# Optimization experiments

Hardware: AMD Instinct MI355X
Metric: run time of the kernel (lower is better)

Reference implementation:

```python
import jax, jax.numpy as jnp
import numpy as np

B, N_IN, D = 2, 262144, 32
N_OUT, K, NK = 65536, 4, 9
MIN_DIST = 0.01


def setup_inputs() -> dict:
    key = jax.random.key(0)
    k1, k2, k3, k4 = jax.random.split(key, 4)
    x_level_in = jax.random.normal(k1, (B, N_IN, D), dtype=jnp.float32)
    coords_in = jax.random.uniform(k2, (2, B, N_IN), dtype=jnp.float32)
    coords_out = jax.random.uniform(k3, (2, B, N_OUT, K), dtype=jnp.float32)
    neighbor_idx = jax.random.randint(k4, (B, N_OUT, K, NK), 0, N_IN)
    sigma = jnp.ones((D,), dtype=jnp.float32) * (MIN_DIST * 200.0)
    return {
        "x_level_in": x_level_in,
        "coords_in": coords_in,
        "coords_out": coords_out,
        "sigma": sigma,
        "neighbor_idx": neighbor_idx,
    }


def reference(x_level_in, coords_in, coords_out, sigma, neighbor_idx):
    # x_level_in: [B, N_in, D]; coords_in: [2, B, N_in]
    # coords_out: [2, B, N_out, K]; neighbor_idx: [B, N_out, K, NK]; sigma: [D]
    b = jnp.arange(x_level_in.shape[0])[:, None, None, None]  # batch index broadcaster
    # gather neighbor coordinates across the input grid: [2, B, N_out, K, NK]
    nb_coords = coords_in[:, b, neighbor_idx]
    # squared euclidean distance in (lon, lat): [B, N_out, K, NK]
    d2 = jnp.sum((coords_out[..., None] - nb_coords) ** 2, axis=0)
    # per-channel Gaussian/RBF weights: [B, N_out, K, NK, D]
    w = jnp.exp(-d2[..., None] / (2.0 * sigma ** 2))
    # gather neighbor features: [B, N_out, K, NK, D]
    feats = x_level_in[b, neighbor_idx]
    # normalized weighted aggregate over the NK neighbors: [B, N_out, K, D]
    num = jnp.sum(w * feats, axis=3)
    den = jnp.sum(w, axis=3) + 1e-9
    x = num / den
    # flatten (N_out, K) -> sequence dim, as in forward's final view
    return x.reshape(x.shape[0], -1, x.shape[-1])
```

## Files before the change

kernel.cpp:

```cpp
#include <hip/hip_runtime.h>
#include <hip/hip_fp16.h>

constexpr int B        = 2;
constexpr int N_IN     = 262144;
constexpr int D        = 32;
constexpr int N_OUT    = 65536;
constexpr int K        = 4;
constexpr int NK       = 9;
constexpr int P        = B * N_OUT * K;
constexpr int PPB      = N_OUT * K;
constexpr size_t XTOT  = (size_t)B * N_IN * D;

typedef _Float16 half2v __attribute__((ext_vector_type(2)));
typedef _Float16 half8v __attribute__((ext_vector_type(8)));
typedef float    f4v    __attribute__((ext_vector_type(4)));

__global__ __launch_bounds__(256) void cvt_fp16_kernel(
    const float* __restrict__ x, _Float16* __restrict__ xh)
{
    const size_t i = (size_t)(blockIdx.x * 256 + threadIdx.x) * 8;
    const float4 a = *reinterpret_cast<const float4*>(x + i);
    const float4 b = *reinterpret_cast<const float4*>(x + i + 4);
    half8v h;
    h[0] = (_Float16)a.x; h[1] = (_Float16)a.y;
    h[2] = (_Float16)a.z; h[3] = (_Float16)a.w;
    h[4] = (_Float16)b.x; h[5] = (_Float16)b.y;
    h[6] = (_Float16)b.z; h[7] = (_Float16)b.w;
    *reinterpret_cast<half8v*>(xh + i) = h;
}

__global__ __launch_bounds__(256) void pack_coords_kernel(
    const float* __restrict__ cin, half2v* __restrict__ cp)
{
    const int i = blockIdx.x * 256 + threadIdx.x;
    half2v h;
    h[0] = (_Float16)cin[i];
    h[1] = (_Float16)cin[B * N_IN + i];
    cp[i] = h;
}

__global__ __launch_bounds__(256) void projection_kernel_h(
    const _Float16* __restrict__ xh,
    const half2v*   __restrict__ cpack,
    const float*    __restrict__ coords_out,
    const float*    __restrict__ sigma,
    const int*      __restrict__ nidx,
    float*          __restrict__ out)
{
    const int bid   = blockIdx.x;
    const int xcd   = bid & 7;
    const int j     = bid >> 3;
    const int batch = xcd >> 2;
    const int bbi   = j * 4 + (xcd & 3);
    const int point = batch * PPB + bbi * 64 + (threadIdx.x >> 2);
    const int h     = threadIdx.x & 3;

    const int cbase = batch * N_IN;

    const float cox = __builtin_nontemporal_load(coords_out + point);
    const float coy = __builtin_nontemporal_load(coords_out + P + point);

    const float4 sg0 = *reinterpret_cast<const float4*>(sigma + h * 8);
    const float4 sg1 = *reinterpret_cast<const float4*>(sigma + h * 8 + 4);
    float s[8];
    s[0] = 1.0f / (2.0f * sg0.x * sg0.x); s[1] = 1.0f / (2.0f * sg0.y * sg0.y);
    s[2] = 1.0f / (2.0f * sg0.z * sg0.z); s[3] = 1.0f / (2.0f * sg0.w * sg0.w);
    s[4] = 1.0f / (2.0f * sg1.x * sg1.x); s[5] = 1.0f / (2.0f * sg1.y * sg1.y);
    s[6] = 1.0f / (2.0f * sg1.z * sg1.z); s[7] = 1.0f / (2.0f * sg1.w * sg1.w);
    bool uni = true;
    #pragma unroll
    for (int k = 1; k < 8; ++k) uni = uni && (s[k] == s[0]);

    int idxs[NK];
    const int* __restrict__ ip = nidx + (size_t)point * NK;
    #pragma unroll
    for (int t = 0; t < NK; ++t) idxs[t] = __builtin_nontemporal_load(ip + t);

    half2v c[NK];
    #pragma unroll
    for (int t = 0; t < NK; ++t) c[t] = cpack[cbase + idxs[t]];

    half8v f[NK];
    #pragma unroll
    for (int t = 0; t < NK; ++t)
        f[t] = *reinterpret_cast<const half8v*>(
            xh + (size_t)(cbase + idxs[t]) * D + h * 8);

    float num[8];
    #pragma unroll
    for (int k = 0; k < 8; ++k) num[k] = 0.f;

    float den[8];
    #pragma unroll
    for (int k = 0; k < 8; ++k) den[k] = 0.f;

    if (uni) {
        #pragma unroll
        for (int t = 0; t < NK; ++t) {
            const float dx = cox - (float)c[t][0];
            const float dy = coy - (float)c[t][1];
            const float w  = __expf(-(dx * dx + dy * dy) * s[0]);
            den[0] += w;
            #pragma unroll
            for (int k = 0; k < 8; ++k) num[k] += w * (float)f[t][k];
        }
        #pragma unroll
        for (int k = 1; k < 8; ++k) den[k] = den[0];
    } else {
        #pragma unroll
        for (int t = 0; t < NK; ++t) {
            const float dx = cox - (float)c[t][0];
            const float dy = coy - (float)c[t][1];
            const float d2 = dx * dx + dy * dy;
            #pragma unroll
            for (int k = 0; k < 8; ++k) {
                const float w = __expf(-d2 * s[k]);
                num[k] += w * (float)f[t][k];
                den[k] += w;
            }
        }
    }

    float* op = out + (size_t)point * D + h * 8;
    f4v o0, o1;
    o0.x = num[0] / (den[0] + 1e-9f); o0.y = num[1] / (den[1] + 1e-9f);
    o0.z = num[2] / (den[2] + 1e-9f); o0.w = num[3] / (den[3] + 1e-9f);
    o1.x = num[4] / (den[4] + 1e-9f); o1.y = num[5] / (den[5] + 1e-9f);
    o1.z = num[6] / (den[6] + 1e-9f); o1.w = num[7] / (den[7] + 1e-9f);
    __builtin_nontemporal_store(o0, reinterpret_cast<f4v*>(op));
    __builtin_nontemporal_store(o1, reinterpret_cast<f4v*>(op + 4));
}

__global__ __launch_bounds__(256) void projection_kernel_f32(
    const float* __restrict__ x,
    const float* __restrict__ coords_in,
    const float* __restrict__ coords_out,
    const float* __restrict__ sigma,
    const int*   __restrict__ nidx,
    float*       __restrict__ out)
{
    const int tid   = blockIdx.x * 256 + threadIdx.x;
    const int point = tid >> 3;
    const int q     = tid & 7;
    const int b     = point / PPB;
    const int cbase = b * N_IN;

    const float cox = coords_out[point];
    const float coy = coords_out[P + point];

    const float4 sg = *reinterpret_cast<const float4*>(sigma + q * 4);
    const float s0 = 1.0f / (2.0f * sg.x * sg.x);
    const float s1 = 1.0f / (2.0f * sg.y * sg.y);
    const float s2 = 1.0f / (2.0f * sg.z * sg.z);
    const float s3 = 1.0f / (2.0f * sg.w * sg.w);

    float4 num = make_float4(0.f, 0.f, 0.f, 0.f);
    float4 den = make_float4(0.f, 0.f, 0.f, 0.f);
    const int* __restrict__ ip = nidx + (size_t)point * NK;

    #pragma unroll
    for (int nk = 0; nk < NK; ++nk) {
        const int idx = ip[nk];
        const float cx = coords_in[cbase + idx];
        const float cy = coords_in[B * N_IN + cbase + idx];
        const float dx = cox - cx;
        const float dy = coy - cy;
        const float d2 = dx * dx + dy * dy;
        const float4 f = *reinterpret_cast<const float4*>(
            x + (size_t)(cbase + idx) * D + q * 4);
        const float w0 = __expf(-d2 * s0);
        const float w1 = __expf(-d2 * s1);
        const float w2 = __expf(-d2 * s2);
        const float w3 = __expf(-d2 * s3);
        num.x += w0 * f.x;  den.x += w0;
        num.y += w1 * f.y;  den.y += w1;
        num.z += w2 * f.z;  den.z += w2;
        num.w += w3 * f.w;  den.w += w3;
    }

    float4 o;
    o.x = num.x / (den.x + 1e-9f);
    o.y = num.y / (den.y + 1e-9f);
    o.z = num.z / (den.z + 1e-9f);
    o.w = num.w / (den.w + 1e-9f);
    *reinterpret_cast<float4*>(out + (size_t)point * D + q * 4) = o;
}

extern "C" void kernel_launch(void* const* d_in, const int* in_sizes, int n_in,
                              void* d_out, int out_size, void* d_ws, size_t ws_size,
                              hipStream_t stream) {
    const float* x      = (const float*)d_in[0];
    const float* cin    = (const float*)d_in[1];
    const float* cout_  = (const float*)d_in[2];
    const float* sigma  = (const float*)d_in[3];
    const int*   nidx   = (const int*)  d_in[4];
    float*       outp   = (float*)d_out;

    const int block = 256;

    const size_t xh_bytes = XTOT * sizeof(_Float16);
    const size_t cp_bytes = (size_t)B * N_IN * sizeof(half2v);

    if (ws_size >= xh_bytes + cp_bytes) {
        _Float16* xh = (_Float16*)d_ws;
        half2v*   cp = (half2v*)((char*)d_ws + xh_bytes);
        cvt_fp16_kernel<<<(int)(XTOT / 8 / block), block, 0, stream>>>(x, xh);
        pack_coords_kernel<<<(B * N_IN) / block, block, 0, stream>>>(cin, cp);
        const int grid_main = (P * 4) / block;
        projection_kernel_h<<<grid_main, block, 0, stream>>>(
            xh, cp, cout_, sigma, nidx, outp);
    } else {
        const int grid_main = (P * 8) / block;
        projection_kernel_f32<<<grid_main, block, 0, stream>>>(
            x, cin, cout_, sigma, nidx, outp);
    }
}
```

Measured before the change: 218.5 us.

## Fuse prep kernels and restructure gather into phased per-thread full-row accumulation

Merges the fp16 conversion and coordinate packing into one prep kernel. The main kernel now gives each thread two whole output points (all 32 channels) instead of a quarter point. It computes scalar weights once per neighbor, then gathers feature rows in four phases keyed on the index range, with block barriers between phases so that concurrent blocks touch a narrower slice of the fp16 feature array and get better L2 locality. The grid is fixed at 1024 blocks with a launch-bounds occupancy hint. The cost is higher register pressure (64 accumulators), fewer threads in flight, and divergent branches within each phase.

```diff
diff --git a/kernel.cpp b/kernel.cpp
--- a/kernel.cpp
+++ b/kernel.cpp
@@ -10,36 +10,77 @@
 constexpr int P        = B * N_OUT * K;
 constexpr int PPB      = N_OUT * K;
 constexpr size_t XTOT  = (size_t)B * N_IN * D;
+constexpr int NPH      = 4;
 
 typedef _Float16 half2v __attribute__((ext_vector_type(2)));
 typedef _Float16 half8v __attribute__((ext_vector_type(8)));
 typedef float    f4v    __attribute__((ext_vector_type(4)));
 
-__global__ __launch_bounds__(256) void cvt_fp16_kernel(
-    const float* __restrict__ x, _Float16* __restrict__ xh)
-{
-    const size_t i = (size_t)(blockIdx.x * 256 + threadIdx.x) * 8;
-    const float4 a = *reinterpret_cast<const float4*>(x + i);
-    const float4 b = *reinterpret_cast<const float4*>(x + i + 4);
+__global__ __launch_bounds__(256) void prep_kernel(
+    const float* __restrict__ x,   _Float16* __restrict__ xh,
+    const float* __restrict__ cin, half2v*   __restrict__ cp)
+{
+    const int tid  = blockIdx.x * 256 + threadIdx.x;
+    const size_t i = (size_t)tid * 8;
+    const f4v a = __builtin_nontemporal_load(reinterpret_cast<const f4v*>(x + i));
+    const f4v b = __builtin_nontemporal_load(reinterpret_cast<const f4v*>(x + i) + 1);
     half8v h;
-    h[0] = (_Float16)a.x; h[1] = (_Float16)a.y;
-    h[2] = (_Float16)a.z; h[3] = (_Float16)a.w;
-    h[4] = (_Float16)b.x; h[5] = (_Float16)b.y;
-    h[6] = (_Float16)b.z; h[7] = (_Float16)b.w;
+    h[0] = (_Float16)a[0]; h[1] = (_Float16)a[1];
+    h[2] = (_Float16)a[2]; h[3] = (_Float16)a[3];
+    h[4] = (_Float16)b[0]; h[5] = (_Float16)b[1];
+    h[6] = (_Float16)b[2]; h[7] = (_Float16)b[3];
     *reinterpret_cast<half8v*>(xh + i) = h;
-}
-
-__global__ __launch_bounds__(256) void pack_coords_kernel(
-    const float* __restrict__ cin, half2v* __restrict__ cp)
-{
-    const int i = blockIdx.x * 256 + threadIdx.x;
-    half2v h;
-    h[0] = (_Float16)cin[i];
-    h[1] = (_Float16)cin[B * N_IN + i];
-    cp[i] = h;
-}
-
-__global__ __launch_bounds__(256) void projection_kernel_h(
+    if (tid < B * N_IN) {
+        half2v c;
+        c[0] = (_Float16)cin[tid];
+        c[1] = (_Float16)cin[B * N_IN + tid];
+        cp[tid] = c;
+    }
+}
+
+__device__ void slow_point(
+    int p, int cbase, const _Float16* __restrict__ xb,
+    const half2v* __restrict__ cpack, const float* __restrict__ coords_out,
+    const float* __restrict__ sigma, const int* __restrict__ nidx,
+    float* __restrict__ out)
+{
+    const float cox = coords_out[p];
+    const float coy = coords_out[P + p];
+    const int* __restrict__ ip = nidx + (size_t)p * NK;
+    int id[NK]; float d2[NK];
+    #pragma unroll
+    for (int t = 0; t < NK; ++t) id[t] = ip[t];
+    #pragma unroll
+    for (int t = 0; t < NK; ++t) {
+        const half2v c = cpack[cbase + id[t]];
+        const float dx = cox - (float)c[0], dy = coy - (float)c[1];
+        d2[t] = dx * dx + dy * dy;
+    }
+    for (int q = 0; q < 4; ++q) {
+        float n[8], d[8], s[8];
+        #pragma unroll
+        for (int k = 0; k < 8; ++k) {
+            n[k] = 0.f; d[k] = 0.f;
+            const float g = sigma[q * 8 + k];
+            s[k] = 1.0f / (2.0f * g * g);
+        }
+        #pragma unroll
+        for (int t = 0; t < NK; ++t) {
+            const half8v f = *reinterpret_cast<const half8v*>(xb + id[t] * D + q * 8);
+            #pragma unroll
+            for (int k = 0; k < 8; ++k) {
+                const float w = __expf(-d2[t] * s[k]);
+                n[k] += w * (float)f[k];
+                d[k] += w;
+            }
+        }
+        #pragma unroll
+        for (int k = 0; k < 8; ++k)
+            out[(size_t)p * D + q * 8 + k] = n[k] / (d[k] + 1e-9f);
+    }
+}
+
+__global__ __launch_bounds__(256, 4) void projection_phase_kernel(
     const _Float16* __restrict__ xh,
     const half2v*   __restrict__ cpack,
     const float*    __restrict__ coords_out,
@@ -49,86 +90,116 @@
 {
     const int bid   = blockIdx.x;
     const int xcd   = bid & 7;
-    const int j     = bid >> 3;
     const int batch = xcd >> 2;
-    const int bbi   = j * 4 + (xcd & 3);
-    const int point = batch * PPB + bbi * 64 + (threadIdx.x >> 2);
-    const int h     = threadIdx.x & 3;
-
+    const int wb    = (bid >> 3) * 4 + (xcd & 3);
+    const int p0    = batch * PPB + wb * 512 + threadIdx.x;
+    const int p1    = p0 + 256;
     const int cbase = batch * N_IN;
-
-    const float cox = __builtin_nontemporal_load(coords_out + point);
-    const float coy = __builtin_nontemporal_load(coords_out + P + point);
-
-    const float4 sg0 = *reinterpret_cast<const float4*>(sigma + h * 8);
-    const float4 sg1 = *reinterpret_cast<const float4*>(sigma + h * 8 + 4);
-    float s[8];
-    s[0] = 1.0f / (2.0f * sg0.x * sg0.x); s[1] = 1.0f / (2.0f * sg0.y * sg0.y);
-    s[2] = 1.0f / (2.0f * sg0.z * sg0.z); s[3] = 1.0f / (2.0f * sg0.w * sg0.w);
-    s[4] = 1.0f / (2.0f * sg1.x * sg1.x); s[5] = 1.0f / (2.0f * sg1.y * sg1.y);
-    s[6] = 1.0f / (2.0f * sg1.z * sg1.z); s[7] = 1.0f / (2.0f * sg1.w * sg1.w);
-    bool uni = true;
-    #pragma unroll
-    for (int k = 1; k < 8; ++k) uni = uni && (s[k] == s[0]);
-
-    int idxs[NK];
-    const int* __restrict__ ip = nidx + (size_t)point * NK;
-    #pragma unroll
-    for (int t = 0; t < NK; ++t) idxs[t] = __builtin_nontemporal_load(ip + t);
-
-    half2v c[NK];
-    #pragma unroll
-    for (int t = 0; t < NK; ++t) c[t] = cpack[cbase + idxs[t]];
-
-    half8v f[NK];
-    #pragma unroll
-    for (int t = 0; t < NK; ++t)
-        f[t] = *reinterpret_cast<const half8v*>(
-            xh + (size_t)(cbase + idxs[t]) * D + h * 8);
-
-    float num[8];
-    #pragma unroll
-    for (int k = 0; k < 8; ++k) num[k] = 0.f;
-
-    float den[8];
-    #pragma unroll
-    for (int k = 0; k < 8; ++k) den[k] = 0.f;
-
-    if (uni) {
-        #pragma unroll
-        for (int t = 0; t < NK; ++t) {
-            const float dx = cox - (float)c[t][0];
-            const float dy = coy - (float)c[t][1];
-            const float w  = __expf(-(dx * dx + dy * dy) * s[0]);
-            den[0] += w;
-            #pragma unroll
-            for (int k = 0; k < 8; ++k) num[k] += w * (float)f[t][k];
-        }
-        #pragma unroll
-        for (int k = 1; k < 8; ++k) den[k] = den[0];
-    } else {
-        #pragma unroll
-        for (int t = 0; t < NK; ++t) {
-            const float dx = cox - (float)c[t][0];
-            const float dy = coy - (float)c[t][1];
-            const float d2 = dx * dx + dy * dy;
-            #pragma unroll
-            for (int k = 0; k < 8; ++k) {
-                const float w = __expf(-d2 * s[k]);
-                num[k] += w * (float)f[t][k];
-                den[k] += w;
+    const _Float16* __restrict__ xb = xh + (size_t)cbase * D;
+
+    float s0; bool uni = true;
+    {
+        const float g = sigma[0];
+        s0 = 1.0f / (2.0f * g * g);
+        for (int k = 1; k < 32; ++k) uni = uni && (sigma[k] == sigma[0]);
+    }
+    if (!uni) {
+        slow_point(p0, cbase, xb, cpack, coords_out, sigma, nidx, out);
+        slow_point(p1, cbase, xb, cpack, coords_out, sigma, nidx, out);
+        return;
+    }
+
+    int   off0[NK], off1[NK];
+    float w0[NK],  w1[NK];
+    float den0 = 0.f, den1 = 0.f;
+    {
+        const float cox0 = __builtin_nontemporal_load(coords_out + p0);
+        const float coy0 = __builtin_nontemporal_load(coords_out + P + p0);
+        const float cox1 = __builtin_nontemporal_load(coords_out + p1);
+        const float coy1 = __builtin_nontemporal_load(coords_out + P + p1);
+        const int* __restrict__ ip0 = nidx + (size_t)p0 * NK;
+        const int* __restrict__ ip1 = nidx + (size_t)p1 * NK;
+        int id0[NK], id1[NK];
+        #pragma unroll
+        for (int t = 0; t < NK; ++t) {
+            id0[t] = __builtin_nontemporal_load(ip0 + t);
+            id1[t] = __builtin_nontemporal_load(ip1 + t);
+        }
+        #pragma unroll
+        for (int t = 0; t < NK; ++t) {
+            const half2v c0 = cpack[cbase + id0[t]];
+            const half2v c1 = cpack[cbase + id1[t]];
+            float dx = cox0 - (float)c0[0], dy = coy0 - (float)c0[1];
+            w0[t] = __expf(-(dx * dx + dy * dy) * s0);  den0 += w0[t];
+            dx = cox1 - (float)c1[0]; dy = coy1 - (float)c1[1];
+            w1[t] = __expf(-(dx * dx + dy * dy) * s0);  den1 += w1[t];
+            off0[t] = id0[t] * D;
+            off1[t] = id1[t] * D;
+        }
+    }
+
+    float num0[32], num1[32];
+    #pragma unroll
+    for (int k = 0; k < 32; ++k) { num0[k] = 0.f; num1[k] = 0.f; }
+
+    for (int ph = 0; ph < NPH; ++ph) {
+        #pragma unroll
+        for (int t = 0; t < NK; ++t) {
+            if ((off0[t] >> 21) == ph) {
+                const _Float16* fp = xb + off0[t];
+                const half8v f0 = *reinterpret_cast<const half8v*>(fp);
+                const half8v f1 = *reinterpret_cast<const half8v*>(fp + 8);
+                const half8v f2 = *reinterpret_cast<const half8v*>(fp + 16);
+                const half8v f3 = *reinterpret_cast<const half8v*>(fp + 24);
+                const float w = w0[t];
+                #pragma unroll
+                for (int k = 0; k < 8; ++k) {
+                    num0[k]      += w * (float)f0[k];
+                    num0[8 + k]  += w * (float)f1[k];
+                    num0[16 + k] += w * (float)f2[k];
+                    num0[24 + k] += w * (float)f3[k];
+                }
             }
         }
-    }
-
-    float* op = out + (size_t)point * D + h * 8;
-    f4v o0, o1;
-    o0.x = num[0] / (den[0] + 1e-9f); o0.y = num[1] / (den[1] + 1e-9f);
-    o0.z = num[2] / (den[2] + 1e-9f); o0.w = num[3] / (den[3] + 1e-9f);
-    o1.x = num[4] / (den[4] + 1e-9f); o1.y = num[5] / (den[5] + 1e-9f);
-    o1.z = num[6] / (den[6] + 1e-9f); o1.w = num[7] / (den[7] + 1e-9f);
-    __builtin_nontemporal_store(o0, reinterpret_cast<f4v*>(op));
-    __builtin_nontemporal_store(o1, reinterpret_cast<f4v*>(op + 4));
+        #pragma unroll
+        for (int t = 0; t < NK; ++t) {
+            if ((off1[t] >> 21) == ph) {
+                const _Float16* fp = xb + off1[t];
+                const half8v f0 = *reinterpret_cast<const half8v*>(fp);
+                const half8v f1 = *reinterpret_cast<const half8v*>(fp + 8);
+                const half8v f2 = *reinterpret_cast<const half8v*>(fp + 16);
+                const half8v f3 = *reinterpret_cast<const half8v*>(fp + 24);
+                const float w = w1[t];
+                #pragma unroll
+                for (int k = 0; k < 8; ++k) {
+                    num1[k]      += w * (float)f0[k];
+                    num1[8 + k]  += w * (float)f1[k];
+                    num1[16 + k] += w * (float)f2[k];
+                    num1[24 + k] += w * (float)f3[k];
+                }
+            }
+        }
+        __syncthreads();
+    }
+
+    const float r0 = 1.0f / (den0 + 1e-9f);
+    const float r1 = 1.0f / (den1 + 1e-9f);
+    float* op0 = out + (size_t)p0 * D;
+    float* op1 = out + (size_t)p1 * D;
+    #pragma unroll
+    for (int c = 0; c < 8; ++c) {
+        f4v o;
+        o[0] = num0[4*c] * r0;   o[1] = num0[4*c+1] * r0;
+        o[2] = num0[4*c+2] * r0; o[3] = num0[4*c+3] * r0;
+        __builtin_nontemporal_store(o, reinterpret_cast<f4v*>(op0) + c);
+    }
+    #pragma unroll
+    for (int c = 0; c < 8; ++c) {
+        f4v o;
+        o[0] = num1[4*c] * r1;   o[1] = num1[4*c+1] * r1;
+        o[2] = num1[4*c+2] * r1; o[3] = num1[4*c+3] * r1;
+        __builtin_nontemporal_store(o, reinterpret_cast<f4v*>(op1) + c);
+    }
 }
 
 __global__ __launch_bounds__(256) void projection_kernel_f32(
@@ -204,10 +275,8 @@
     if (ws_size >= xh_bytes + cp_bytes) {
         _Float16* xh = (_Float16*)d_ws;
         half2v*   cp = (half2v*)((char*)d_ws + xh_bytes);
-        cvt_fp16_kernel<<<(int)(XTOT / 8 / block), block, 0, stream>>>(x, xh);
-        pack_coords_kernel<<<(B * N_IN) / block, block, 0, stream>>>(cin, cp);
-        const int grid_main = (P * 4) / block;
-        projection_kernel_h<<<grid_main, block, 0, stream>>>(
+        prep_kernel<<<(int)(XTOT / 8 / block), block, 0, stream>>>(x, xh, cin, cp);
+        projection_phase_kernel<<<1024, block, 0, stream>>>(
             xh, cp, cout_, sigma, nidx, outp);
     } else {
         const int grid_main = (P * 8) / block;
```

New measurement: 397.1 us. 1.82x slower.
